# Kernel tuning notes

Measured on AMD Instinct MI355X. Metric: run time of the kernel, lower is better.

The kernel has to match this reference:

```python
import jax, jax.numpy as jnp
import numpy as np

N, E = 50000, 600000
DIN, D, C = 239, 128, 2
NEG_SLOPE_MLP = 0.01   # nn.LeakyReLU default
NEG_SLOPE_ATT = 0.2    # GATConv default


def leaky(x, s):
    return jnp.where(x >= 0, x, s * x)


def setup_inputs() -> dict:
    key = jax.random.key(0)
    ks = jax.random.split(key, 12)
    sc = lambda d: 1.0 / np.sqrt(d)
    return {
        "x": jax.random.normal(ks[0], (N, DIN), jnp.float32),
        "edge_index": jax.random.randint(ks[1], (2, E), 0, N, jnp.int32),
        "edge_type": jax.random.randint(ks[2], (E,), 0, 4, jnp.int32),
        "W_in": jax.random.normal(ks[3], (DIN, D), jnp.float32) * sc(DIN),
        "b_in": jnp.zeros((D,), jnp.float32),
        "W_gat": jax.random.normal(ks[4], (D, D), jnp.float32) * sc(D),
        "att_src": jax.random.normal(ks[5], (D,), jnp.float32) * sc(D),
        "att_dst": jax.random.normal(ks[6], (D,), jnp.float32) * sc(D),
        "b_gat": jnp.zeros((D,), jnp.float32),
        "W_h": jax.random.normal(ks[7], (D, D), jnp.float32) * sc(D),
        "b_h": jnp.zeros((D,), jnp.float32),
        "W_out": jax.random.normal(ks[8], (D, C), jnp.float32) * sc(D),
        "b_out": jnp.zeros((C,), jnp.float32),
    }


def reference(x, edge_index, edge_type, W_in, b_in, W_gat, att_src, att_dst,
              b_gat, W_h, b_h, W_out, b_out):
    # input encoder: Linear + LeakyReLU
    h = leaky(x @ W_in + b_in, NEG_SLOPE_MLP)                      # [N, D]

    # GATConv (heads=1): add self loops, edge attention, segment softmax over dst
    loops = jnp.arange(N, dtype=edge_index.dtype)
    src = jnp.concatenate([edge_index[0], loops])                  # [E+N]
    dst = jnp.concatenate([edge_index[1], loops])

    g = h @ W_gat                                                  # [N, D]
    a_src = g @ att_src                                            # [N]
    a_dst = g @ att_dst                                            # [N]
    e = leaky(a_src[src] + a_dst[dst], NEG_SLOPE_ATT)              # [E+N]

    m = jax.ops.segment_max(e, dst, num_segments=N)                # self-loops => no empty segs
    w = jnp.exp(e - m[dst])
    z = jax.ops.segment_sum(w, dst, num_segments=N)
    alpha = w / z[dst]                                             # [E+N]

    out = jax.ops.segment_sum(alpha[:, None] * g[src], dst, num_segments=N) + b_gat

    # dropout is identity in eval mode
    h2 = leaky(out @ W_h + b_h, NEG_SLOPE_MLP)
    return h2 @ W_out + b_out                                      # [N, C]
```

## Files before the change

kernel.cpp:

```cpp
#include <hip/hip_runtime.h>

#define NNODE 50000
#define NEDGE 600000
#define KDIN  239
#define DDIM  128
#define NTILES 3125
#define NBG   782
#define NBUCK 256
#define BSZ   196
#define HBSZ  98
#define NPB   128
#define CHP   4688
#define ESCAP 4096

typedef _Float16 half8 __attribute__((ext_vector_type(8)));
typedef _Float16 half4 __attribute__((ext_vector_type(4)));
typedef __attribute__((ext_vector_type(4))) float f32x4;

__device__ __forceinline__ ushort f2h(float f){
  union { _Float16 h; ushort u; } c; c.h = (_Float16)f; return c.u;
}

__global__ __launch_bounds__(256) void pre_k(
    const float* __restrict__ W_in, const float* __restrict__ W_gat, const float* __restrict__ W_h,
    ushort* __restrict__ BfA, ushort* __restrict__ BfB, ushort* __restrict__ BfC,
    const int* __restrict__ ei, int* __restrict__ cpart)
{
  __shared__ int hb[NBUCK];
  const int b = blockIdx.x, t = threadIdx.x;
  if (b < NPB){
    hb[t] = 0;
    __syncthreads();
    const int e0 = b*CHP, e1 = min(NEDGE, e0+CHP);
    for (int e=e0+t; e<e1; e+=256){
      int dst = min(max(ei[NEDGE+e],0), NNODE-1);
      atomicAdd(&hb[dst/BSZ], 1);
    }
    __syncthreads();
    cpart[b*NBUCK + t] = hb[t];
  } else if (b < NPB + 128){
    int idx = (b-NPB)*256 + t; int n = idx >> 8, k = idx & 255;
    BfA[idx] = (k < KDIN) ? f2h(W_in[(size_t)k*DDIM + n]) : (ushort)0;
  } else if (b < NPB + 192){
    int idx = (b-NPB-128)*256 + t; int n = idx >> 7, k = idx & 127;
    BfB[idx] = f2h(W_gat[(size_t)k*DDIM + n]);
  } else {
    int idx = (b-NPB-192)*256 + t; int n = idx >> 7, k = idx & 127;
    BfC[idx] = f2h(W_h[(size_t)k*DDIM + n]);
  }
}

__global__ __launch_bounds__(256, 3) void gemmAB_k(
    const float* __restrict__ x, const ushort* __restrict__ BfA,
    const ushort* __restrict__ BfB, const float* __restrict__ b_in,
    ushort* __restrict__ gf,
    const float* __restrict__ vs, const float* __restrict__ vd,
    float* __restrict__ os, float* __restrict__ od,
    float* __restrict__ bms, float* __restrict__ bmd,
    const int* __restrict__ ei, const int* __restrict__ cpart, int* __restrict__ pairs,
    int* __restrict__ gmS)
{
  __shared__ __attribute__((aligned(16))) ushort Bs[128*128];
  __shared__ __attribute__((aligned(16))) ushort ht[4][16*128];
  if (blockIdx.x < NPB){
    int* cur = (int*)Bs;
    int* scn = ((int*)Bs) + NBUCK;
    const int pb = blockIdx.x, t = threadIdx.x;
    int tot = 0, before = 0;
    #pragma unroll 8
    for (int i=0;i<NPB;i++){
      const int c = cpart[i*NBUCK + t];
      if (i < pb) before += c;
      tot += c;
    }
    scn[t] = tot;
    __syncthreads();
    #pragma unroll
    for (int off=1; off<NBUCK; off<<=1){
      int v = (t>=off) ? scn[t-off] : 0;
      __syncthreads();
      scn[t] += v;
      __syncthreads();
    }
    const int S = scn[t] - tot;
    cur[t] = S + before;
    if (pb == 0) gmS[t] = S;
    __syncthreads();
    const int e0 = pb*CHP, e1 = min(NEDGE, e0+CHP);
    for (int e=e0+t; e<e1; e+=256){
      int dst = min(max(ei[NEDGE+e],0), NNODE-1);
      int src = min(max(ei[e],0), NNODE-1);
      int bk = (unsigned)dst / BSZ;
      int pos = atomicAdd(&cur[bk], 1);
      pairs[pos] = src | ((dst - bk*BSZ) << 16);
    }
    return;
  }
  const int lane = threadIdx.x & 63;
  const int wave = threadIdx.x >> 6;
  const int q = lane >> 4, c = lane & 15;
  const int tile = (blockIdx.x - NPB)*4 + wave;
  const bool act = tile < NTILES;
  const int rowBase = tile*16;
  const int swz = (c&7)<<4;
  f32x4 acc[8];
  half8 af[8];
  if (act){
    const float* __restrict__ ap = x + (size_t)(rowBase + c)*KDIN;
    #pragma unroll
    for (int s=0;s<7;s++){
      const float* __restrict__ p = ap + s*32 + q*8;
      #pragma unroll
      for (int i=0;i<8;i++) af[s][i] = (_Float16)p[i];
    }
    #pragma unroll
    for (int i=0;i<8;i++){
      const int k = 224 + q*8 + i;
      af[7][i] = (_Float16)((k < KDIN) ? ap[k] : 0.f);
    }
    #pragma unroll
    for (int t=0;t<8;t++) acc[t] = (f32x4){0.f,0.f,0.f,0.f};
  }
  #pragma unroll
  for (int H=0; H<2; ++H){
    #pragma unroll
    for (int it=0; it<8; ++it){
      const int idx = it*256 + threadIdx.x;
      const int row = idx >> 4, sl = (idx & 15)*16;
      const half8 v = *(const half8*)(BfA + (size_t)row*256 + H*128 + (idx & 15)*8);
      *(half8*)((char*)Bs + row*256 + (sl ^ ((row&7)<<4))) = v;
    }
    __syncthreads();
    if (act){
      const char* __restrict__ bsl = (const char*)Bs + c*256;
      #pragma unroll
      for (int s=0;s<4;s++){
        const int so = (s*64 + q*16) ^ swz;
        #pragma unroll
        for (int t=0;t<8;t++){
          const half8 bf = *(const half8*)(bsl + t*16*256 + so);
          acc[t] = __builtin_amdgcn_mfma_f32_16x16x32_f16(af[H*4+s], bf, acc[t], 0,0,0);
        }
      }
    }
    __syncthreads();
  }
  if (act){
    char* __restrict__ hw = (char*)&ht[wave][0];
    #pragma unroll
    for (int t=0;t<8;t++){
      const int col = 16*t + c;
      const float bv = b_in[col];
      #pragma unroll
      for (int r=0;r<4;r++){
        const int row = q*4 + r;
        float v = acc[t][r] + bv;
        v = (v >= 0.f) ? v : 0.01f*v;
        *(_Float16*)(hw + ((row*256 + col*2) ^ ((row&7)<<4))) = (_Float16)v;
      }
    }
  }
  #pragma unroll
  for (int it=0; it<8; ++it){
    const int idx = it*256 + threadIdx.x;
    const int row = idx >> 4, sl = (idx & 15)*16;
    const half8 v = *(const half8*)(BfB + (size_t)idx*8);
    *(half8*)((char*)Bs + row*256 + (sl ^ ((row&7)<<4))) = v;
  }
  __syncthreads();
  if (!act) return;
  half8 af2[4];
  const char* __restrict__ hr = (const char*)&ht[wave][0] + c*256;
  #pragma unroll
  for (int s=0;s<4;s++) af2[s] = *(const half8*)(hr + ((s*64 + q*16) ^ swz));
  #pragma unroll
  for (int t=0;t<8;t++) acc[t] = (f32x4){0.f,0.f,0.f,0.f};
  const char* __restrict__ bsl2 = (const char*)Bs + c*256;
  #pragma unroll
  for (int s=0;s<4;s++){
    const int so = (s*64 + q*16) ^ swz;
    #pragma unroll
    for (int t=0;t<8;t++){
      const half8 bf = *(const half8*)(bsl2 + t*16*256 + so);
      acc[t] = __builtin_amdgcn_mfma_f32_16x16x32_f16(af2[s], bf, acc[t], 0,0,0);
    }
  }
  float pr0[4] = {0,0,0,0}, pr1[4] = {0,0,0,0};
  #pragma unroll
  for (int t=0;t<8;t++){
    const int col = 16*t + c;
    const float va = vs[col], vb = vd[col];
    #pragma unroll
    for (int r=0;r<4;r++){
      const int row = rowBase + q*4 + r;
      const float v = acc[t][r];
      gf[(size_t)row*DDIM + col] = f2h(v);
      pr0[r] += v*va; pr1[r] += v*vb;
    }
  }
  float lmax_s = -3.0e38f, lmax_d = -3.0e38f;
  #pragma unroll
  for (int r=0;r<4;r++){
    float s0 = pr0[r], s1 = pr1[r];
    s0 += __shfl_xor(s0,8); s1 += __shfl_xor(s1,8);
    s0 += __shfl_xor(s0,4); s1 += __shfl_xor(s1,4);
    s0 += __shfl_xor(s0,2); s1 += __shfl_xor(s1,2);
    s0 += __shfl_xor(s0,1); s1 += __shfl_xor(s1,1);
    lmax_s = fmaxf(lmax_s, s0); lmax_d = fmaxf(lmax_d, s1);
    if (c == 0){
      const int row = rowBase + q*4 + r;
      os[row] = s0; od[row] = s1;
    }
  }
  #pragma unroll
  for (int off=32; off>0; off>>=1){
    lmax_s = fmaxf(lmax_s, __shfl_xor(lmax_s, off));
    lmax_d = fmaxf(lmax_d, __shfl_xor(lmax_d, off));
  }
  if (lane == 0){ bms[tile] = lmax_s; bmd[tile] = lmax_d; }
}

__global__ __launch_bounds__(1024, 2) void fineagg_k(
    const int* __restrict__ pairs, const int* __restrict__ gmS,
    int* __restrict__ es, const ushort* __restrict__ gf,
    const float* __restrict__ a_src, const float* __restrict__ a_dst,
    const float* __restrict__ bms, const float* __restrict__ bmd,
    const float* __restrict__ b_gat, ushort* __restrict__ og)
{
  __shared__ int fh[256];
  __shared__ int sc2[256];
  __shared__ int offL[256];
  __shared__ int degL[256];
  __shared__ int esL[ESCAP];
  __shared__ float Msh;
  const int b = blockIdx.x >> 1;
  const int hf2 = blockIdx.x & 1;
  const int t = threadIdx.x;
  float ms = -3.0e38f, md = -3.0e38f;
  for (int i=t; i<NTILES; i+=1024){ ms = fmaxf(ms, bms[i]); md = fmaxf(md, bmd[i]); }
  #pragma unroll
  for (int off=32; off>0; off>>=1){
    ms = fmaxf(ms, __shfl_xor(ms, off));
    md = fmaxf(md, __shfl_xor(md, off));
  }
  float* red = (float*)sc2;
  const int w = t >> 6;
  if ((t & 63) == 0){ red[w] = ms; red[16+w] = md; }
  __syncthreads();
  if (t == 0){
    float As = red[0], Ad = red[16];
    #pragma unroll
    for (int i=1;i<16;i++){ As = fmaxf(As, red[i]); Ad = fmaxf(Ad, red[16+i]); }
    float M = As + Ad;
    Msh = (M >= 0.f) ? M : 0.2f*M;
  }
  if (t < 256) fh[t] = 0;
  __syncthreads();
  const int s0 = gmS[b];
  const int s1 = (b < NBUCK-1) ? gmS[b+1] : NEDGE;
  const bool fit = (s1 - s0) <= ESCAP;
  for (int i=s0+t; i<s1; i+=1024)
    atomicAdd(&fh[pairs[i] >> 16], 1);
  __syncthreads();
  int deg = 0;
  if (t < 256){ deg = fh[t]; sc2[t] = deg; }
  __syncthreads();
  #pragma unroll
  for (int off=1; off<256; off<<=1){
    int v = (t < 256 && t >= off) ? sc2[t-off] : 0;
    __syncthreads();
    if (t < 256) sc2[t] += v;
    __syncthreads();
  }
  if (t < 256){
    const int excl = sc2[t] - deg;
    offL[t] = excl;
    degL[t] = deg;
    fh[t] = excl;
  }
  __syncthreads();
  for (int i=s0+t; i<s1; i+=1024){
    const int p = pairs[i];
    const int pos = atomicAdd(&fh[p >> 16], 1);
    if (fit) esL[pos] = p & 0xFFFF;
    else if (hf2 == 0) es[s0 + pos] = p & 0xFFFF;
  }
  __syncthreads();
  const float M = Msh;
  const int lane = t & 63;
  const int half = lane >> 5, li = lane & 31;
  const int slot = (t >> 6)*2 + half;
  const int D0 = hf2*HBSZ, D1 = hf2 ? BSZ : HBSZ;
  const float4 bg = *(const float4*)&b_gat[li*4];
  for (int d = D0 + slot; d < D1; d += 32){
    const int dst = b*BSZ + d;
    if (dst >= NNODE) continue;
    const float ad = a_dst[dst];
    f32x4 a0={0,0,0,0}, a1={0,0,0,0}, a2={0,0,0,0}, a3={0,0,0,0};
    float w0s=0.f, w1s=0.f, w2s=0.f, w3s=0.f;
    if (fit){
      const int start = offL[d];
      const int dg = degL[d];
      const int* __restrict__ bin = esL + start;
      int j = 0;
      for (; j+3 < dg; j += 4){
        const int i0=bin[j], i1=bin[j+1], i2=bin[j+2], i3=bin[j+3];
        float e0=a_src[i0]+ad; e0=(e0>=0.f)?e0:0.2f*e0;
        float e1=a_src[i1]+ad; e1=(e1>=0.f)?e1:0.2f*e1;
        float e2=a_src[i2]+ad; e2=(e2>=0.f)?e2:0.2f*e2;
        float e3=a_src[i3]+ad; e3=(e3>=0.f)?e3:0.2f*e3;
        const float w0=__expf(e0-M), w1=__expf(e1-M), w2=__expf(e2-M), w3=__expf(e3-M);
        const half4 g0 = *(const half4*)(gf + (size_t)i0*DDIM + li*4);
        const half4 g1 = *(const half4*)(gf + (size_t)i1*DDIM + li*4);
        const half4 g2 = *(const half4*)(gf + (size_t)i2*DDIM + li*4);
        const half4 g3 = *(const half4*)(gf + (size_t)i3*DDIM + li*4);
        #pragma unroll
        for (int i=0;i<4;i++){
          a0[i] += w0*(float)g0[i]; a1[i] += w1*(float)g1[i];
          a2[i] += w2*(float)g2[i]; a3[i] += w3*(float)g3[i];
        }
        w0s += w0; w1s += w1; w2s += w2; w3s += w3;
      }
      for (; j < dg; ++j){
        const int si = bin[j];
        float e0=a_src[si]+ad; e0=(e0>=0.f)?e0:0.2f*e0;
        const float w = __expf(e0-M);
        const half4 gv = *(const half4*)(gf + (size_t)si*DDIM + li*4);
        #pragma unroll
        for (int i=0;i<4;i++) a0[i] += w*(float)gv[i];
        w0s += w;
      }
    } else {
      for (int i=s0; i<s1; ++i){
        const int p = pairs[i];
        if ((p >> 16) != d) continue;
        const int si = p & 0xFFFF;
        float e0=a_src[si]+ad; e0=(e0>=0.f)?e0:0.2f*e0;
        const float w = __expf(e0-M);
        const half4 gv = *(const half4*)(gf + (size_t)si*DDIM + li*4);
        #pragma unroll
        for (int i2v=0;i2v<4;i2v++) a0[i2v] += w*(float)gv[i2v];
        w0s += w;
      }
    }
    {
      float evs=a_src[dst]+ad; evs=(evs>=0.f)?evs:0.2f*evs;
      const float w = __expf(evs-M);
      const half4 gv = *(const half4*)(gf + (size_t)dst*DDIM + li*4);
      #pragma unroll
      for (int i=0;i<4;i++) a0[i] += w*(float)gv[i];
      w0s += w;
    }
    const float inv = 1.f/(w0s+w1s+w2s+w3s);
    ushort4 o;
    o.x = f2h((a0[0]+a1[0]+a2[0]+a3[0])*inv + bg.x);
    o.y = f2h((a0[1]+a1[1]+a2[1]+a3[1])*inv + bg.y);
    o.z = f2h((a0[2]+a1[2]+a2[2]+a3[2])*inv + bg.z);
    o.w = f2h((a0[3]+a1[3]+a2[3]+a3[3])*inv + bg.w);
    *(ushort4*)(og + (size_t)dst*DDIM + li*4) = o;
  }
}

__global__ __launch_bounds__(256, 4) void gemmC_k(
    const ushort* __restrict__ Af, const ushort* __restrict__ Btf,
    const float* __restrict__ bias, float* __restrict__ outf,
    const float* __restrict__ Wo, const float* __restrict__ bo)
{
  constexpr int Kpad = 128, Kb = 256;
  __shared__ __attribute__((aligned(16))) ushort Bs[128*Kpad];
  #pragma unroll
  for (int it=0; it<8; ++it){
    const int idx = it*256 + threadIdx.x;
    const int row = idx >> 4, sl = (idx & 15)*16;
    const half8 v = *(const half8*)(Btf + (size_t)idx*8);
    *(half8*)((char*)Bs + row*Kb + (sl ^ ((row&7)<<4))) = v;
  }
  __syncthreads();
  const int lane = threadIdx.x & 63;
  const int wave = threadIdx.x >> 6;
  const int q = lane >> 4, c = lane & 15;
  const int tile = blockIdx.x*4 + wave;
  if (tile >= NTILES) return;
  const int rowBase = tile*16;
  half8 af[4];
  const ushort* __restrict__ ap = Af + (size_t)(rowBase + c)*Kpad + q*8;
  #pragma unroll
  for (int s=0;s<4;s++) af[s] = *(const half8*)(ap + s*32);
  f32x4 acc[8];
  #pragma unroll
  for (int t=0;t<8;t++) acc[t] = (f32x4){0.f,0.f,0.f,0.f};
  const int swz = (c&7)<<4;
  const char* __restrict__ bsl = (const char*)Bs + c*Kb;
  #pragma unroll
  for (int s=0;s<4;s++){
    const int so = (s*64 + q*16) ^ swz;
    #pragma unroll
    for (int t=0;t<8;t++){
      const half8 bf = *(const half8*)(bsl + t*16*Kb + so);
      acc[t] = __builtin_amdgcn_mfma_f32_16x16x32_f16(af[s], bf, acc[t], 0,0,0);
    }
  }
  float pr0[4] = {0,0,0,0}, pr1[4] = {0,0,0,0};
  #pragma unroll
  for (int t=0;t<8;t++){
    const int col = 16*t + c;
    const float bv = bias[col];
    const float va = Wo[2*col], vb = Wo[2*col+1];
    #pragma unroll
    for (int r=0;r<4;r++){
      float v = acc[t][r] + bv;
      v = (v >= 0.f) ? v : 0.01f*v;
      pr0[r] += v*va; pr1[r] += v*vb;
    }
  }
  #pragma unroll
  for (int r=0;r<4;r++){
    float s0 = pr0[r], s1 = pr1[r];
    s0 += __shfl_xor(s0,8); s1 += __shfl_xor(s1,8);
    s0 += __shfl_xor(s0,4); s1 += __shfl_xor(s1,4);
    s0 += __shfl_xor(s0,2); s1 += __shfl_xor(s1,2);
    s0 += __shfl_xor(s0,1); s1 += __shfl_xor(s1,1);
    if (c == 0){
      const int row = rowBase + q*4 + r;
      float2 y2; y2.x = s0 + bo[0]; y2.y = s1 + bo[1];
      *(float2*)&outf[(size_t)row*2] = y2;
    }
  }
}

extern "C" void kernel_launch(void* const* d_in, const int* in_sizes, int n_in,
                              void* d_out, int out_size, void* d_ws, size_t ws_size,
                              hipStream_t stream)
{
  const float* x       = (const float*)d_in[0];
  const int*   ei      = (const int*)d_in[1];
  const float* W_in    = (const float*)d_in[3];
  const float* b_in    = (const float*)d_in[4];
  const float* W_gat   = (const float*)d_in[5];
  const float* att_src = (const float*)d_in[6];
  const float* att_dst = (const float*)d_in[7];
  const float* b_gat   = (const float*)d_in[8];
  const float* W_h     = (const float*)d_in[9];
  const float* b_h     = (const float*)d_in[10];
  const float* W_out   = (const float*)d_in[11];
  const float* b_out   = (const float*)d_in[12];

  char* ws = (char*)d_ws;
  ushort*   gf     = (ushort*)  (ws + 0);
  ushort*   og     = (ushort*)  (ws + 12800000);
  ushort*   BfA    = (ushort*)  (ws + 25600000);
  ushort*   BfB    = (ushort*)  (ws + 25800000);
  ushort*   BfC    = (ushort*)  (ws + 25900000);
  int*      cpart  = (int*)     (ws + 26000000);
  int*      pairs  = (int*)     (ws + 26300000);
  int*      es     = (int*)     (ws + 28700000);
  float*    a_src  = (float*)   (ws + 31100000);
  float*    a_dst  = (float*)   (ws + 31300000);
  int*      gmS    = (int*)     (ws + 31500000);
  float*    bmaxS  = (float*)   (ws + 31600000);
  float*    bmaxD  = (float*)   (ws + 31616000);

  pre_k<<<NPB + 256, 256, 0, stream>>>(W_in, W_gat, W_h, BfA, BfB, BfC, ei, cpart);
  gemmAB_k<<<NPB + NBG, 256, 0, stream>>>(x, BfA, BfB, b_in, gf,
      att_src, att_dst, a_src, a_dst, bmaxS, bmaxD, ei, cpart, pairs, gmS);
  fineagg_k<<<2*NBUCK, 1024, 0, stream>>>(pairs, gmS, es, gf, a_src, a_dst,
      bmaxS, bmaxD, b_gat, og);
  gemmC_k<<<NBG, 256, 0, stream>>>(og, BfC, b_h, (float*)d_out, W_out, b_out);
}
```

Before: 167.3 us.

## Fuse final GEMM into aggregation kernel and switch to power-of-two dst buckets

The final W_h GEMM and output projection now run inside the aggregation kernel. Each block aggregates 64 destination rows into shared memory as fp16, then runs MFMA against W_h, which is staged in two halves reusing the edge-list buffer. This removes the og round trip through global memory and one kernel launch. Buckets change to 256 nodes each so indexing uses shifts and masks, and each bucket is split across four blocks. The risks are that the edge list is now rescanned by four blocks per bucket, and the global-memory fallback for overflowing buckets is dropped in favour of a slow linear scan of pairs.

```diff
diff --git a/kernel.cpp b/kernel.cpp
--- a/kernel.cpp
+++ b/kernel.cpp
@@ -6,12 +6,12 @@
 #define DDIM  128
 #define NTILES 3125
 #define NBG   782
-#define NBUCK 256
-#define BSZ   196
-#define HBSZ  98
+#define NBUCK 196
+#define BSZ   256
+#define QSZ   64
 #define NPB   128
 #define CHP   4688
-#define ESCAP 4096
+#define ESCAP 6144
 
 typedef _Float16 half8 __attribute__((ext_vector_type(8)));
 typedef _Float16 half4 __attribute__((ext_vector_type(4)));
@@ -26,7 +26,7 @@
     ushort* __restrict__ BfA, ushort* __restrict__ BfB, ushort* __restrict__ BfC,
     const int* __restrict__ ei, int* __restrict__ cpart)
 {
-  __shared__ int hb[NBUCK];
+  __shared__ int hb[256];
   const int b = blockIdx.x, t = threadIdx.x;
   if (b < NPB){
     hb[t] = 0;
@@ -34,10 +34,10 @@
     const int e0 = b*CHP, e1 = min(NEDGE, e0+CHP);
     for (int e=e0+t; e<e1; e+=256){
       int dst = min(max(ei[NEDGE+e],0), NNODE-1);
-      atomicAdd(&hb[dst/BSZ], 1);
-    }
-    __syncthreads();
-    cpart[b*NBUCK + t] = hb[t];
+      atomicAdd(&hb[dst>>8], 1);
+    }
+    __syncthreads();
+    cpart[b*256 + t] = hb[t];
   } else if (b < NPB + 128){
     int idx = (b-NPB)*256 + t; int n = idx >> 8, k = idx & 255;
     BfA[idx] = (k < KDIN) ? f2h(W_in[(size_t)k*DDIM + n]) : (ushort)0;
@@ -64,19 +64,19 @@
   __shared__ __attribute__((aligned(16))) ushort ht[4][16*128];
   if (blockIdx.x < NPB){
     int* cur = (int*)Bs;
-    int* scn = ((int*)Bs) + NBUCK;
+    int* scn = ((int*)Bs) + 256;
     const int pb = blockIdx.x, t = threadIdx.x;
     int tot = 0, before = 0;
     #pragma unroll 8
     for (int i=0;i<NPB;i++){
-      const int c = cpart[i*NBUCK + t];
+      const int c = cpart[i*256 + t];
       if (i < pb) before += c;
       tot += c;
     }
     scn[t] = tot;
     __syncthreads();
     #pragma unroll
-    for (int off=1; off<NBUCK; off<<=1){
+    for (int off=1; off<256; off<<=1){
       int v = (t>=off) ? scn[t-off] : 0;
       __syncthreads();
       scn[t] += v;
@@ -90,9 +90,9 @@
     for (int e=e0+t; e<e1; e+=256){
       int dst = min(max(ei[NEDGE+e],0), NNODE-1);
       int src = min(max(ei[e],0), NNODE-1);
-      int bk = (unsigned)dst / BSZ;
+      int bk = (unsigned)dst >> 8;
       int pos = atomicAdd(&cur[bk], 1);
-      pairs[pos] = src | ((dst - bk*BSZ) << 16);
+      pairs[pos] = src | ((dst & 255) << 16);
     }
     return;
   }
@@ -222,19 +222,22 @@
 
 __global__ __launch_bounds__(1024, 2) void fineagg_k(
     const int* __restrict__ pairs, const int* __restrict__ gmS,
-    int* __restrict__ es, const ushort* __restrict__ gf,
+    const ushort* __restrict__ gf,
     const float* __restrict__ a_src, const float* __restrict__ a_dst,
     const float* __restrict__ bms, const float* __restrict__ bmd,
-    const float* __restrict__ b_gat, ushort* __restrict__ og)
+    const float* __restrict__ b_gat, const ushort* __restrict__ BfC,
+    const float* __restrict__ b_h, const float* __restrict__ Wo,
+    const float* __restrict__ bo, float* __restrict__ outf)
 {
   __shared__ int fh[256];
   __shared__ int sc2[256];
   __shared__ int offL[256];
   __shared__ int degL[256];
-  __shared__ int esL[ESCAP];
+  __shared__ __attribute__((aligned(16))) int esL[ESCAP];
+  __shared__ __attribute__((aligned(16))) ushort ogL[QSZ*128];
   __shared__ float Msh;
-  const int b = blockIdx.x >> 1;
-  const int hf2 = blockIdx.x & 1;
+  const int b = blockIdx.x >> 2;
+  const int qtr = blockIdx.x & 3;
   const int t = threadIdx.x;
   float ms = -3.0e38f, md = -3.0e38f;
   for (int i=t; i<NTILES; i+=1024){ ms = fmaxf(ms, bms[i]); md = fmaxf(md, bmd[i]); }
@@ -279,28 +282,29 @@
     fh[t] = excl;
   }
   __syncthreads();
-  for (int i=s0+t; i<s1; i+=1024){
-    const int p = pairs[i];
-    const int pos = atomicAdd(&fh[p >> 16], 1);
-    if (fit) esL[pos] = p & 0xFFFF;
-    else if (hf2 == 0) es[s0 + pos] = p & 0xFFFF;
+  if (fit){
+    for (int i=s0+t; i<s1; i+=1024){
+      const int p = pairs[i];
+      const int pos = atomicAdd(&fh[p >> 16], 1);
+      esL[pos] = p & 0xFFFF;
+    }
   }
   __syncthreads();
   const float M = Msh;
   const int lane = t & 63;
   const int half = lane >> 5, li = lane & 31;
   const int slot = (t >> 6)*2 + half;
-  const int D0 = hf2*HBSZ, D1 = hf2 ? BSZ : HBSZ;
   const float4 bg = *(const float4*)&b_gat[li*4];
-  for (int d = D0 + slot; d < D1; d += 32){
-    const int dst = b*BSZ + d;
+  for (int sl = slot; sl < QSZ; sl += 32){
+    const int doff = qtr*QSZ + sl;
+    const int dst = b*BSZ + doff;
     if (dst >= NNODE) continue;
     const float ad = a_dst[dst];
     f32x4 a0={0,0,0,0}, a1={0,0,0,0}, a2={0,0,0,0}, a3={0,0,0,0};
     float w0s=0.f, w1s=0.f, w2s=0.f, w3s=0.f;
     if (fit){
-      const int start = offL[d];
-      const int dg = degL[d];
+      const int start = offL[doff];
+      const int dg = degL[doff];
       const int* __restrict__ bin = esL + start;
       int j = 0;
       for (; j+3 < dg; j += 4){
@@ -324,106 +328,119 @@
       for (; j < dg; ++j){
         const int si = bin[j];
         float e0=a_src[si]+ad; e0=(e0>=0.f)?e0:0.2f*e0;
-        const float w = __expf(e0-M);
+        const float w2v = __expf(e0-M);
         const half4 gv = *(const half4*)(gf + (size_t)si*DDIM + li*4);
         #pragma unroll
-        for (int i=0;i<4;i++) a0[i] += w*(float)gv[i];
-        w0s += w;
+        for (int i=0;i<4;i++) a0[i] += w2v*(float)gv[i];
+        w0s += w2v;
       }
     } else {
       for (int i=s0; i<s1; ++i){
         const int p = pairs[i];
-        if ((p >> 16) != d) continue;
+        if ((p >> 16) != doff) continue;
         const int si = p & 0xFFFF;
         float e0=a_src[si]+ad; e0=(e0>=0.f)?e0:0.2f*e0;
-        const float w = __expf(e0-M);
+        const float w2v = __expf(e0-M);
         const half4 gv = *(const half4*)(gf + (size_t)si*DDIM + li*4);
         #pragma unroll
-        for (int i2v=0;i2v<4;i2v++) a0[i2v] += w*(float)gv[i2v];
-        w0s += w;
+        for (int i2v=0;i2v<4;i2v++) a0[i2v] += w2v*(float)gv[i2v];
+        w0s += w2v;
       }
     }
     {
       float evs=a_src[dst]+ad; evs=(evs>=0.f)?evs:0.2f*evs;
-      const float w = __expf(evs-M);
+      const float w2v = __expf(evs-M);
       const half4 gv = *(const half4*)(gf + (size_t)dst*DDIM + li*4);
       #pragma unroll
-      for (int i=0;i<4;i++) a0[i] += w*(float)gv[i];
-      w0s += w;
+      for (int i=0;i<4;i++) a0[i] += w2v*(float)gv[i];
+      w0s += w2v;
     }
     const float inv = 1.f/(w0s+w1s+w2s+w3s);
-    ushort4 o;
-    o.x = f2h((a0[0]+a1[0]+a2[0]+a3[0])*inv + bg.x);
-    o.y = f2h((a0[1]+a1[1]+a2[1]+a3[1])*inv + bg.y);
-    o.z = f2h((a0[2]+a1[2]+a2[2]+a3[2])*inv + bg.z);
-    o.w = f2h((a0[3]+a1[3]+a2[3]+a3[3])*inv + bg.w);
-    *(ushort4*)(og + (size_t)dst*DDIM + li*4) = o;
-  }
-}
-
-__global__ __launch_bounds__(256, 4) void gemmC_k(
-    const ushort* __restrict__ Af, const ushort* __restrict__ Btf,
-    const float* __restrict__ bias, float* __restrict__ outf,
-    const float* __restrict__ Wo, const float* __restrict__ bo)
-{
-  constexpr int Kpad = 128, Kb = 256;
-  __shared__ __attribute__((aligned(16))) ushort Bs[128*Kpad];
-  #pragma unroll
-  for (int it=0; it<8; ++it){
-    const int idx = it*256 + threadIdx.x;
-    const int row = idx >> 4, sl = (idx & 15)*16;
-    const half8 v = *(const half8*)(Btf + (size_t)idx*8);
-    *(half8*)((char*)Bs + row*Kb + (sl ^ ((row&7)<<4))) = v;
-  }
-  __syncthreads();
-  const int lane = threadIdx.x & 63;
-  const int wave = threadIdx.x >> 6;
+    half4 o;
+    o[0] = (_Float16)((a0[0]+a1[0]+a2[0]+a3[0])*inv + bg.x);
+    o[1] = (_Float16)((a0[1]+a1[1]+a2[1]+a3[1])*inv + bg.y);
+    o[2] = (_Float16)((a0[2]+a1[2]+a2[2]+a3[2])*inv + bg.z);
+    o[3] = (_Float16)((a0[3]+a1[3]+a2[3]+a3[3])*inv + bg.w);
+    const int tw = sl >> 4, row16 = sl & 15;
+    *(half4*)((char*)ogL + tw*4096 + ((row16*256 + li*8) ^ ((row16&7)<<4))) = o;
+  }
+  __syncthreads();
+  ushort* Bc = (ushort*)esL;
+  {
+    const int row = t >> 4, sl16 = (t & 15)*16;
+    const half8 v = *(const half8*)(BfC + (size_t)row*128 + (t & 15)*8);
+    *(half8*)((char*)Bc + row*256 + (sl16 ^ ((row&7)<<4))) = v;
+  }
+  __syncthreads();
   const int q = lane >> 4, c = lane & 15;
-  const int tile = blockIdx.x*4 + wave;
-  if (tile >= NTILES) return;
-  const int rowBase = tile*16;
+  const int swz = (c&7)<<4;
+  const bool mw = w < 4;
+  f32x4 acc[8];
   half8 af[4];
-  const ushort* __restrict__ ap = Af + (size_t)(rowBase + c)*Kpad + q*8;
-  #pragma unroll
-  for (int s=0;s<4;s++) af[s] = *(const half8*)(ap + s*32);
-  f32x4 acc[8];
-  #pragma unroll
-  for (int t=0;t<8;t++) acc[t] = (f32x4){0.f,0.f,0.f,0.f};
-  const int swz = (c&7)<<4;
-  const char* __restrict__ bsl = (const char*)Bs + c*Kb;
-  #pragma unroll
-  for (int s=0;s<4;s++){
-    const int so = (s*64 + q*16) ^ swz;
-    #pragma unroll
-    for (int t=0;t<8;t++){
-      const half8 bf = *(const half8*)(bsl + t*16*Kb + so);
-      acc[t] = __builtin_amdgcn_mfma_f32_16x16x32_f16(af[s], bf, acc[t], 0,0,0);
+  if (mw){
+    const char* __restrict__ ap = (const char*)ogL + w*4096 + c*256;
+    #pragma unroll
+    for (int s=0;s<4;s++) af[s] = *(const half8*)(ap + ((s*64 + q*16) ^ swz));
+    #pragma unroll
+    for (int u=0;u<8;u++) acc[u] = (f32x4){0.f,0.f,0.f,0.f};
+    const char* __restrict__ bsl = (const char*)Bc + c*256;
+    #pragma unroll
+    for (int s=0;s<4;s++){
+      const int so = (s*64 + q*16) ^ swz;
+      #pragma unroll
+      for (int u=0;u<4;u++){
+        const half8 bf = *(const half8*)(bsl + u*16*256 + so);
+        acc[u] = __builtin_amdgcn_mfma_f32_16x16x32_f16(af[s], bf, acc[u], 0,0,0);
+      }
+    }
+  }
+  __syncthreads();
+  {
+    const int row = t >> 4, sl16 = (t & 15)*16;
+    const half8 v = *(const half8*)(BfC + (size_t)(row+64)*128 + (t & 15)*8);
+    *(half8*)((char*)Bc + row*256 + (sl16 ^ ((row&7)<<4))) = v;
+  }
+  __syncthreads();
+  if (!mw) return;
+  {
+    const char* __restrict__ bsl = (const char*)Bc + c*256;
+    #pragma unroll
+    for (int s=0;s<4;s++){
+      const int so = (s*64 + q*16) ^ swz;
+      #pragma unroll
+      for (int u=0;u<4;u++){
+        const half8 bf = *(const half8*)(bsl + u*16*256 + so);
+        acc[4+u] = __builtin_amdgcn_mfma_f32_16x16x32_f16(af[s], bf, acc[4+u], 0,0,0);
+      }
     }
   }
   float pr0[4] = {0,0,0,0}, pr1[4] = {0,0,0,0};
   #pragma unroll
-  for (int t=0;t<8;t++){
-    const int col = 16*t + c;
-    const float bv = bias[col];
+  for (int v8=0;v8<8;v8++){
+    const int col = 16*v8 + c;
+    const float bv = b_h[col];
     const float va = Wo[2*col], vb = Wo[2*col+1];
     #pragma unroll
     for (int r=0;r<4;r++){
-      float v = acc[t][r] + bv;
+      float v = acc[v8][r] + bv;
       v = (v >= 0.f) ? v : 0.01f*v;
       pr0[r] += v*va; pr1[r] += v*vb;
     }
   }
+  const int rowBase = b*BSZ + qtr*QSZ + w*16;
   #pragma unroll
   for (int r=0;r<4;r++){
-    float s0 = pr0[r], s1 = pr1[r];
-    s0 += __shfl_xor(s0,8); s1 += __shfl_xor(s1,8);
-    s0 += __shfl_xor(s0,4); s1 += __shfl_xor(s1,4);
-    s0 += __shfl_xor(s0,2); s1 += __shfl_xor(s1,2);
-    s0 += __shfl_xor(s0,1); s1 += __shfl_xor(s1,1);
+    float s0v = pr0[r], s1v = pr1[r];
+    s0v += __shfl_xor(s0v,8); s1v += __shfl_xor(s1v,8);
+    s0v += __shfl_xor(s0v,4); s1v += __shfl_xor(s1v,4);
+    s0v += __shfl_xor(s0v,2); s1v += __shfl_xor(s1v,2);
+    s0v += __shfl_xor(s0v,1); s1v += __shfl_xor(s1v,1);
     if (c == 0){
       const int row = rowBase + q*4 + r;
-      float2 y2; y2.x = s0 + bo[0]; y2.y = s1 + bo[1];
-      *(float2*)&outf[(size_t)row*2] = y2;
+      if (row < NNODE){
+        float2 y2; y2.x = s0v + bo[0]; y2.y = s1v + bo[1];
+        *(float2*)&outf[(size_t)row*2] = y2;
+      }
     }
   }
 }
@@ -447,23 +464,20 @@
 
   char* ws = (char*)d_ws;
   ushort*   gf     = (ushort*)  (ws + 0);
-  ushort*   og     = (ushort*)  (ws + 12800000);
-  ushort*   BfA    = (ushort*)  (ws + 25600000);
-  ushort*   BfB    = (ushort*)  (ws + 25800000);
-  ushort*   BfC    = (ushort*)  (ws + 25900000);
-  int*      cpart  = (int*)     (ws + 26000000);
-  int*      pairs  = (int*)     (ws + 26300000);
-  int*      es     = (int*)     (ws + 28700000);
-  float*    a_src  = (float*)   (ws + 31100000);
-  float*    a_dst  = (float*)   (ws + 31300000);
-  int*      gmS    = (int*)     (ws + 31500000);
-  float*    bmaxS  = (float*)   (ws + 31600000);
-  float*    bmaxD  = (float*)   (ws + 31616000);
+  ushort*   BfA    = (ushort*)  (ws + 12800000);
+  ushort*   BfB    = (ushort*)  (ws + 13000000);
+  ushort*   BfC    = (ushort*)  (ws + 13100000);
+  int*      cpart  = (int*)     (ws + 13200000);
+  int*      pairs  = (int*)     (ws + 13500000);
+  float*    a_src  = (float*)   (ws + 15900000);
+  float*    a_dst  = (float*)   (ws + 16100000);
+  int*      gmS    = (int*)     (ws + 16300000);
+  float*    bmaxS  = (float*)   (ws + 16400000);
+  float*    bmaxD  = (float*)   (ws + 16416000);
 
   pre_k<<<NPB + 256, 256, 0, stream>>>(W_in, W_gat, W_h, BfA, BfB, BfC, ei, cpart);
   gemmAB_k<<<NPB + NBG, 256, 0, stream>>>(x, BfA, BfB, b_in, gf,
       att_src, att_dst, a_src, a_dst, bmaxS, bmaxD, ei, cpart, pairs, gmS);
-  fineagg_k<<<2*NBUCK, 1024, 0, stream>>>(pairs, gmS, es, gf, a_src, a_dst,
-      bmaxS, bmaxD, b_gat, og);
-  gemmC_k<<<NBG, 256, 0, stream>>>(og, BfC, b_h, (float*)d_out, W_out, b_out);
+  fineagg_k<<<4*NBUCK, 1024, 0, stream>>>(pairs, gmS, gf, a_src, a_dst,
+      bmaxS, bmaxD, b_gat, BfC, b_h, W_out, b_out, (float*)d_out);
 }
```

After: 189.7 us. 13.4% more time.
